# Performance work log

Hardware: AMD Instinct MI355X
Metric: run time of the kernel (lower is better)

## Reference

```python
import jax, jax.numpy as jnp
import numpy as np

B, S, E = 4, 4096, 1024
HEADS, WINDOW = 16, 128
HEAD_DIM = E // HEADS


def setup_inputs() -> dict:
    key = jax.random.key(0)
    ks = jax.random.split(key, 6)
    x = jax.random.normal(ks[0], (B, S, E), dtype=jnp.float32)
    attn_mask = jnp.ones((B, 1, S), dtype=jnp.float32)
    scale = 1.0 / np.sqrt(E)
    Wq = jax.random.normal(ks[1], (E, E), dtype=jnp.float32) * scale
    Wk = jax.random.normal(ks[2], (E, E), dtype=jnp.float32) * scale
    Wv = jax.random.normal(ks[3], (E, E), dtype=jnp.float32) * scale
    Wo = jax.random.normal(ks[4], (E, E), dtype=jnp.float32) * scale
    return {"x": x, "attn_mask": attn_mask, "Wq": Wq, "Wk": Wk, "Wv": Wv, "Wo": Wo}


def _look_around(t, axis_windows=2):
    # t: [..., nw, w, ...]; returns concat of windows [i-1, i, i+1] along the
    # intra-window axis, zero-padded at the boundaries.
    pad = [(0, 0)] * t.ndim
    pad[axis_windows] = (1, 1)
    tp = jnp.pad(t, pad)
    nw = t.shape[axis_windows]
    def sl(start):
        idx = [slice(None)] * t.ndim
        idx[axis_windows] = slice(start, start + nw)
        return tp[tuple(idx)]
    return jnp.concatenate([sl(0), sl(1), sl(2)], axis=axis_windows + 1)


def _local_attention(q, k, v, key_mask, window):
    # q,k,v: [b, h, n, d]; key_mask: [b, n] bool. Non-causal, look_backward=1,
    # look_forward=1 (lucidrains LocalAttention defaults for causal=False).
    b, h, n, d = q.shape
    nw = n // window
    scale = d ** -0.5
    qb = q.reshape(b, h, nw, window, d) * scale
    kb = k.reshape(b, h, nw, window, d)
    vb = v.reshape(b, h, nw, window, d)
    k_look = _look_around(kb, axis_windows=2)  # [b,h,nw,3w,d]
    v_look = _look_around(vb, axis_windows=2)
    # mask: user key mask AND in-bounds (padded boundary windows are invalid)
    mb = key_mask.reshape(b, nw, window)
    m_look = _look_around(mb, axis_windows=1)  # [b,nw,3w]
    m_look = m_look[:, None, :, None, :]       # [b,1,nw,1,3w]
    scores = jnp.einsum('bhnwd,bhnkd->bhnwk', qb, k_look)
    mask_value = -jnp.finfo(scores.dtype).max
    scores = jnp.where(m_look, scores, mask_value)
    attn = jax.nn.softmax(scores, axis=-1)
    out = jnp.einsum('bhnwk,bhnkd->bhnwd', attn, v_look)
    return out.reshape(b, h, n, d)


def reference(x, attn_mask, Wq, Wk, Wv, Wo):
    b, c, e = x.shape
    h, d = HEADS, HEAD_DIM
    q = jnp.einsum('bce,ef->bcf', x, Wq.T).reshape(b, c, h, d).transpose(0, 2, 1, 3)
    k = jnp.einsum('bce,ef->bcf', x, Wk.T).reshape(b, c, h, d).transpose(0, 2, 1, 3)
    v = jnp.einsum('bce,ef->bcf', x, Wv.T).reshape(b, c, h, d).transpose(0, 2, 1, 3)
    key_mask = attn_mask[:, 0, :] > 0  # [b, c] bool
    attended = _local_attention(q, k, v, key_mask, WINDOW)
    attended = attended.transpose(0, 2, 1, 3).reshape(b, c, h * d)
    return jnp.einsum('bcf,fe->bce', attended, Wo.T)
```

## Files before the change

kernel.cpp:

```cpp
#include <hip/hip_runtime.h>
#include <stdint.h>

typedef __bf16 bf16_t;
typedef __bf16 bf16x8 __attribute__((ext_vector_type(8)));
typedef __bf16 bf16x4 __attribute__((ext_vector_type(4)));
typedef float f32x4 __attribute__((ext_vector_type(4)));

__device__ __forceinline__ f32x4 mfma16(bf16x8 a, bf16x8 b, f32x4 c) {
  return __builtin_amdgcn_mfma_f32_16x16x32_bf16(a, b, c, 0, 0, 0);
}

__device__ __forceinline__ void g2l16(const void* g, void* l) {
  __builtin_amdgcn_global_load_lds((const __attribute__((address_space(1))) void*)g,
                                   (__attribute__((address_space(3))) void*)l, 16, 0, 0);
}

#define FENCE() asm volatile("" ::: "memory")

__global__ void __launch_bounds__(256) cvt_f32_bf16(const float* __restrict__ in,
                                                    bf16_t* __restrict__ out) {
  long i = ((long)blockIdx.x * 256 + threadIdx.x) * 8;
  float4 f0 = *(const float4*)(in + i);
  float4 f1 = *(const float4*)(in + i + 4);
  bf16x8 v;
  v[0] = (bf16_t)f0.x; v[1] = (bf16_t)f0.y; v[2] = (bf16_t)f0.z; v[3] = (bf16_t)f0.w;
  v[4] = (bf16_t)f1.x; v[5] = (bf16_t)f1.y; v[6] = (bf16_t)f1.z; v[7] = (bf16_t)f1.w;
  *(bf16x8*)(out + i) = v;
}

template <typename OutT>
__global__ void __launch_bounds__(512, 2) gemm256(const bf16_t* __restrict__ A,
                                                  const bf16_t* __restrict__ Bt,
                                                  OutT* __restrict__ C,
                                                  int M, int N, int K, int NBN) {
  extern __shared__ char smem[];
  const int t = threadIdx.x;
  const int w = t >> 6, l = t & 63;
  const int lr = l & 15, lg = l >> 4;
  const int wm = w >> 2, wn = w & 3;

  const int nwg = gridDim.x;
  const int flat = blockIdx.x;
  const int swz = (flat & 7) * (nwg >> 3) + (flat >> 3);
  const int bm = swz / NBN, bn = swz % NBN;
  const long rowA0 = (long)bm * 256;
  const long colC0 = (long)bn * 256;
  const int KT = K >> 6;

  const int colSwz = ((l & 7) ^ (l >> 3)) * 8;
  const bf16_t* gA = A + (rowA0 + w * 32 + (l >> 3)) * (long)K + colSwz;
  const bf16_t* gB = Bt + (colC0 + w * 32 + (l >> 3)) * (long)K + colSwz;
  const long K8 = (long)K * 8;

  const int sx0 = (lg ^ (lr & 7)) * 16;
  const int sx1 = ((4 + lg) ^ (lr & 7)) * 16;
  const int aRow = (wm * 128 + lr) * 128;
  const int bRow = 32768 + (wn * 64 + lr) * 128;

  f32x4 acc[8][4] = {};

#define STAGE_A(buf, kt)                                          \
  {                                                               \
    char* _d = smem + (buf) * 65536 + w * 4096;                   \
    const long _ko = (long)(kt) * 64;                             \
    g2l16(gA + _ko, _d);                                          \
    g2l16(gA + K8 + _ko, _d + 1024);                              \
    g2l16(gA + 2 * K8 + _ko, _d + 2048);                          \
    g2l16(gA + 3 * K8 + _ko, _d + 3072);                          \
  }
#define STAGE_B(buf, kt)                                          \
  {                                                               \
    char* _d = smem + (buf) * 65536 + 32768 + w * 4096;           \
    const long _ko = (long)(kt) * 64;                             \
    g2l16(gB + _ko, _d);                                          \
    g2l16(gB + K8 + _ko, _d + 1024);                              \
    g2l16(gB + 2 * K8 + _ko, _d + 2048);                          \
    g2l16(gB + 3 * K8 + _ko, _d + 3072);                          \
  }

  STAGE_A(0, 0); STAGE_B(0, 0);
  FENCE();
  asm volatile("s_waitcnt vmcnt(0)" ::: "memory");
  __builtin_amdgcn_s_barrier();

  for (int kt = 0; kt < KT; ++kt) {
    const char* sb = smem + (kt & 1) * 65536;
    const int nb = (kt + 1) & 1;
    const bool ds = (kt + 1) < KT;

    bf16x8 bfr[4][2];

    {
      bf16x8 a0[4][2];
#pragma unroll
      for (int j = 0; j < 4; ++j) {
        bfr[j][0] = *(const bf16x8*)(sb + bRow + j * 2048 + sx0);
        bfr[j][1] = *(const bf16x8*)(sb + bRow + j * 2048 + sx1);
      }
#pragma unroll
      for (int i = 0; i < 4; ++i) {
        a0[i][0] = *(const bf16x8*)(sb + aRow + i * 2048 + sx0);
        a0[i][1] = *(const bf16x8*)(sb + aRow + i * 2048 + sx1);
      }
      if (ds) STAGE_A(nb, kt + 1);
      FENCE();
      __builtin_amdgcn_s_barrier();
      asm volatile("s_waitcnt lgkmcnt(0)" ::: "memory");
      __builtin_amdgcn_sched_barrier(0);
      __builtin_amdgcn_s_setprio(1);
#pragma unroll
      for (int i = 0; i < 4; ++i)
#pragma unroll
        for (int j = 0; j < 4; ++j) {
          acc[i][j] = mfma16(a0[i][0], bfr[j][0], acc[i][j]);
          acc[i][j] = mfma16(a0[i][1], bfr[j][1], acc[i][j]);
        }
      __builtin_amdgcn_s_setprio(0);
      __builtin_amdgcn_sched_barrier(0);
      FENCE();
      __builtin_amdgcn_s_barrier();
    }

    {
      bf16x8 a1[4][2];
#pragma unroll
      for (int i = 0; i < 4; ++i) {
        a1[i][0] = *(const bf16x8*)(sb + aRow + (4 + i) * 2048 + sx0);
        a1[i][1] = *(const bf16x8*)(sb + aRow + (4 + i) * 2048 + sx1);
      }
      if (ds) STAGE_B(nb, kt + 1);
      FENCE();
      __builtin_amdgcn_s_barrier();
      asm volatile("s_waitcnt lgkmcnt(0)" ::: "memory");
      __builtin_amdgcn_sched_barrier(0);
      __builtin_amdgcn_s_setprio(1);
#pragma unroll
      for (int i = 0; i < 4; ++i)
#pragma unroll
        for (int j = 0; j < 4; ++j) {
          acc[4 + i][j] = mfma16(a1[i][0], bfr[j][0], acc[4 + i][j]);
          acc[4 + i][j] = mfma16(a1[i][1], bfr[j][1], acc[4 + i][j]);
        }
      __builtin_amdgcn_s_setprio(0);
      __builtin_amdgcn_sched_barrier(0);
      FENCE();
      if (ds) {
        asm volatile("s_waitcnt vmcnt(0)" ::: "memory");
      }
      __builtin_amdgcn_s_barrier();
    }
  }

#pragma unroll
  for (int i = 0; i < 8; ++i)
#pragma unroll
    for (int j = 0; j < 4; ++j)
#pragma unroll
      for (int r = 0; r < 4; ++r) {
        long row = rowA0 + wm * 128 + i * 16 + lg * 4 + r;
        long col = colC0 + wn * 64 + j * 16 + lr;
        C[row * (long)N + col] = (OutT)acc[i][j][r];
      }
#undef STAGE_A
#undef STAGE_B
}

__global__ void __launch_bounds__(512, 4) swa3(const bf16_t* __restrict__ QK,
                                               const bf16_t* __restrict__ VT,
                                               const float* __restrict__ amask,
                                               bf16_t* __restrict__ Att) {
  extern __shared__ char lds[];
  bf16_t* Ks = (bf16_t*)lds;
  bf16_t* Vs = (bf16_t*)(lds + 16384);
  float* bias = (float*)(lds + 32768);
  const int t = threadIdx.x, w = t >> 6, l = t & 63, lr = l & 15, lg = l >> 4;
  char* Psw = lds + 34304 + w * 4352;

  const int idx = (blockIdx.x & 7) * 256 + (blockIdx.x >> 3);
  const int n = idx & 31, h = (idx >> 5) & 15, b = idx >> 9;
  const long rowQ = (long)b * 4096 + n * 128;

  bf16x8 qf[2];
#pragma unroll
  for (int ks = 0; ks < 2; ++ks)
    qf[ks] = *(const bf16x8*)&QK[(rowQ + w * 16 + lr) * 2048 + h * 64 + ks * 32 + lg * 8];

  f32x4 oT[4] = {};
  float m_run = -1e30f, l_run = 0.f;

  const int kcLo = (n > 0) ? n - 1 : 0;
  const int kcHi = (n < 31) ? n + 1 : 31;
  const long kbase0 = (long)b * 4096 + (long)kcLo * 128;
  const int nch = kcHi - kcLo + 1;

  const int kcol = ((t & 7) ^ ((t >> 3) & 7)) * 8;
  const bf16_t* gK0 = QK + (kbase0 + (t >> 3)) * 2048 + 1024 + h * 64 + kcol;
  const int vrow = t >> 4;
  const int vcol = ((t & 15) ^ ((t >> 4) & 15)) * 8;
  const bf16_t* gV0 = VT + ((long)h * 64 + vrow) * 16384 + kbase0 + vcol;

  bf16_t* lK0 = Ks + t * 8;
  bf16_t* lK1 = Ks + 4096 + t * 8;
  bf16_t* lV0 = Vs + t * 8;
  bf16_t* lV1 = Vs + 4096 + t * 8;

#define STAGE_K(cc)                                               \
  {                                                               \
    const bf16_t* _k = gK0 + (long)(cc) * 128 * 2048;             \
    g2l16(_k, lK0);                                               \
    g2l16(_k + (long)64 * 2048, lK1);                             \
  }
#define STAGE_V(cc)                                               \
  {                                                               \
    const bf16_t* _v = gV0 + (long)(cc) * 128;                    \
    g2l16(_v, lV0);                                               \
    g2l16(_v + (long)32 * 16384, lV1);                            \
  }

  STAGE_K(0); STAGE_V(0);
  if (t < nch * 32) {
    float4 mv = *(const float4*)(amask + kbase0 + t * 4);
    float4 bv;
    bv.x = mv.x > 0.f ? 0.f : -1e30f;
    bv.y = mv.y > 0.f ? 0.f : -1e30f;
    bv.z = mv.z > 0.f ? 0.f : -1e30f;
    bv.w = mv.w > 0.f ? 0.f : -1e30f;
    *(float4*)&bias[t * 4] = bv;
  }
  FENCE();
  asm volatile("s_waitcnt vmcnt(0)" ::: "memory");
  __syncthreads();

  for (int c = 0; c < nch; ++c) {
    const bool more = (c + 1) < nch;

    f32x4 s[8];
#pragma unroll
    for (int kb = 0; kb < 8; ++kb) {
      f32x4 z = {};
#pragma unroll
      for (int ks = 0; ks < 2; ++ks) {
        bf16x8 kA = *(const bf16x8*)&Ks[(kb * 16 + lr) * 64 + (((ks * 4 + lg) ^ (lr & 7)) * 8)];
        z = mfma16(kA, qf[ks], z);
      }
      s[kb] = z;
    }
    FENCE();
    __builtin_amdgcn_s_barrier();
    if (more) STAGE_K(c + 1);

    float mt = -3e30f;
#pragma unroll
    for (int kb = 0; kb < 8; ++kb) {
      f32x4 bb = *(const f32x4*)&bias[c * 128 + kb * 16 + lg * 4];
#pragma unroll
      for (int r = 0; r < 4; ++r) {
        float sv = s[kb][r] * 0.125f + bb[r];
        s[kb][r] = sv;
        mt = fmaxf(mt, sv);
      }
    }
    mt = fmaxf(mt, __shfl_xor(mt, 16));
    mt = fmaxf(mt, __shfl_xor(mt, 32));
    float mnew = fmaxf(m_run, mt);
    float alpha = __expf(m_run - mnew);
    m_run = mnew;
    float rs = 0.f;
#pragma unroll
    for (int kb = 0; kb < 8; ++kb)
#pragma unroll
      for (int r = 0; r < 4; ++r) {
        float p = __expf(s[kb][r] - mnew);
        s[kb][r] = p;
        rs += p;
      }
    rs += __shfl_xor(rs, 16);
    rs += __shfl_xor(rs, 32);
    l_run = l_run * alpha + rs;
#pragma unroll
    for (int df = 0; df < 4; ++df)
#pragma unroll
      for (int r = 0; r < 4; ++r) oT[df][r] *= alpha;

#pragma unroll
    for (int kb = 0; kb < 8; ++kb) {
      bf16x4 pv;
      pv[0] = (bf16_t)s[kb][0]; pv[1] = (bf16_t)s[kb][1];
      pv[2] = (bf16_t)s[kb][2]; pv[3] = (bf16_t)s[kb][3];
      *(bf16x4*)(Psw + lr * 272 + kb * 32 + lg * 8) = pv;
    }
    asm volatile("s_waitcnt lgkmcnt(0)" ::: "memory");
    __builtin_amdgcn_sched_barrier(0);

    FENCE();
    if (more) asm volatile("s_waitcnt vmcnt(2)" ::: "memory");
    else      asm volatile("s_waitcnt vmcnt(0)" ::: "memory");
    __builtin_amdgcn_s_barrier();

#pragma unroll
    for (int ks = 0; ks < 4; ++ks) {
      bf16x8 pB = *(const bf16x8*)(Psw + lr * 272 + ks * 64 + lg * 16);
#pragma unroll
      for (int df = 0; df < 4; ++df) {
        bf16x8 vA = *(const bf16x8*)&Vs[(df * 16 + lr) * 128 + (((ks * 4 + lg) ^ lr) * 8)];
        oT[df] = mfma16(vA, pB, oT[df]);
      }
    }
    FENCE();
    __builtin_amdgcn_s_barrier();
    if (more) {
      STAGE_V(c + 1);
      FENCE();
      asm volatile("s_waitcnt vmcnt(2)" ::: "memory");
      __builtin_amdgcn_s_barrier();
    }
  }
#undef STAGE_K
#undef STAGE_V

  float inv = 1.f / l_run;
#pragma unroll
  for (int df = 0; df < 4; ++df) {
    bf16x4 ov;
#pragma unroll
    for (int r = 0; r < 4; ++r) ov[r] = (bf16_t)(oT[df][r] * inv);
    *(bf16x4*)(Psw + lr * 272 + df * 32 + lg * 8) = ov;
  }
  asm volatile("s_waitcnt lgkmcnt(0)" ::: "memory");
  __builtin_amdgcn_sched_barrier(0);
  const char* myP = lds + 34304 + w * 4352;
  bf16x8 r0 = *(const bf16x8*)(myP + (l >> 2) * 272 + (l & 3) * 32);
  bf16x8 r1 = *(const bf16x8*)(myP + (l >> 2) * 272 + (l & 3) * 32 + 16);
  long orow = rowQ + w * 16 + (l >> 2);
  bf16_t* op = Att + orow * 1024 + h * 64 + (l & 3) * 16;
  *(bf16x8*)op = r0;
  *(bf16x8*)(op + 8) = r1;
}

extern "C" void kernel_launch(void* const* d_in, const int* in_sizes, int n_in,
                              void* d_out, int out_size, void* d_ws, size_t ws_size,
                              hipStream_t stream) {
  const float* x  = (const float*)d_in[0];
  const float* am = (const float*)d_in[1];
  const float* Wq = (const float*)d_in[2];
  const float* Wk = (const float*)d_in[3];
  const float* Wv = (const float*)d_in[4];
  const float* Wo = (const float*)d_in[5];
  float* out = (float*)d_out;

  char* ws = (char*)d_ws;
  bf16_t* qk  = (bf16_t*)ws;
  bf16_t* vt  = (bf16_t*)(ws + 67108864);
  bf16_t* xbx = (bf16_t*)(ws + 100663296);
  bf16_t* wqk = (bf16_t*)(ws + 134217728);
  bf16_t* wvb = (bf16_t*)(ws + 138412032);
  bf16_t* wob = (bf16_t*)(ws + 140509184);

  const int kSmemG = 131072;
  hipFuncSetAttribute(reinterpret_cast<const void*>(&gemm256<bf16_t>),
                      hipFuncAttributeMaxDynamicSharedMemorySize, kSmemG);
  hipFuncSetAttribute(reinterpret_cast<const void*>(&gemm256<float>),
                      hipFuncAttributeMaxDynamicSharedMemorySize, kSmemG);
  const int kSmemS = 69120;
  hipFuncSetAttribute(reinterpret_cast<const void*>(&swa3),
                      hipFuncAttributeMaxDynamicSharedMemorySize, kSmemS);

  cvt_f32_bf16<<<8192, 256, 0, stream>>>(x, xbx);
  cvt_f32_bf16<<<512, 256, 0, stream>>>(Wq, wqk);
  cvt_f32_bf16<<<512, 256, 0, stream>>>(Wk, wqk + 1048576);
  cvt_f32_bf16<<<512, 256, 0, stream>>>(Wv, wvb);
  cvt_f32_bf16<<<512, 256, 0, stream>>>(Wo, wob);

  gemm256<bf16_t><<<512, 512, kSmemG, stream>>>(xbx, wqk, qk, 16384, 2048, 1024, 8);

  gemm256<bf16_t><<<256, 512, kSmemG, stream>>>(wvb, xbx, vt, 1024, 16384, 1024, 64);

  swa3<<<2048, 512, kSmemS, stream>>>(qk, vt, am, xbx);

  gemm256<float><<<256, 512, kSmemG, stream>>>(xbx, wob, out, 16384, 1024, 1024, 4);
}
```

Before: 229.7 us.

## Use triple-buffered K=32 LDS pipeline in GEMM with two tiles in flight

Rewrites the bf16 GEMM main loop from a double-buffered K=64 stage, split into two half-phases, to a three-slot ring of K=32 stages, prefetching two tiles ahead with vmcnt-based partial waits. Each iteration loads all A/B fragments once and issues 32 MFMAs between barriers. The goal is to hide global-load latency better and cut LDS from 128KB to 96KB. In exchange it has twice as many iterations, so barrier overhead per unit of work goes up, and a new swizzle pattern could change LDS bank conflicts.

```diff
diff --git a/kernel.cpp b/kernel.cpp
--- a/kernel.cpp
+++ b/kernel.cpp
@@ -29,10 +29,10 @@
 }
 
 template <typename OutT>
-__global__ void __launch_bounds__(512, 2) gemm256(const bf16_t* __restrict__ A,
-                                                  const bf16_t* __restrict__ Bt,
-                                                  OutT* __restrict__ C,
-                                                  int M, int N, int K, int NBN) {
+__global__ void __launch_bounds__(512, 2) gemm3r(const bf16_t* __restrict__ A,
+                                                 const bf16_t* __restrict__ Bt,
+                                                 OutT* __restrict__ C,
+                                                 int M, int N, int K, int NBN) {
   extern __shared__ char smem[];
   const int t = threadIdx.x;
   const int w = t >> 6, l = t & 63;
@@ -45,111 +45,66 @@
   const int bm = swz / NBN, bn = swz % NBN;
   const long rowA0 = (long)bm * 256;
   const long colC0 = (long)bn * 256;
-  const int KT = K >> 6;
-
-  const int colSwz = ((l & 7) ^ (l >> 3)) * 8;
-  const bf16_t* gA = A + (rowA0 + w * 32 + (l >> 3)) * (long)K + colSwz;
-  const bf16_t* gB = Bt + (colC0 + w * 32 + (l >> 3)) * (long)K + colSwz;
-  const long K8 = (long)K * 8;
-
-  const int sx0 = (lg ^ (lr & 7)) * 16;
-  const int sx1 = ((4 + lg) ^ (lr & 7)) * 16;
-  const int aRow = (wm * 128 + lr) * 128;
-  const int bRow = 32768 + (wn * 64 + lr) * 128;
+  const int KT = K >> 5;
+
+  const int colSwz = (((t & 3) ^ ((t >> 2) & 3))) * 8;
+  const bf16_t* gA = A + (rowA0 + (t >> 2)) * (long)K + colSwz;
+  const bf16_t* gB = Bt + (colC0 + (t >> 2)) * (long)K + colSwz;
+  const long K128 = (long)K * 128;
+
+  const int sxa = (lg ^ (lr & 3)) * 16;
+  const int aRow = (wm * 128 + lr) * 64;
+  const int bRow = 16384 + (wn * 64 + lr) * 64;
 
   f32x4 acc[8][4] = {};
 
-#define STAGE_A(buf, kt)                                          \
+#define STAGE(slot, kt)                                           \
   {                                                               \
-    char* _d = smem + (buf) * 65536 + w * 4096;                   \
-    const long _ko = (long)(kt) * 64;                             \
+    char* _d = smem + (slot) * 32768 + t * 16;                    \
+    const long _ko = (long)(kt) * 32;                             \
     g2l16(gA + _ko, _d);                                          \
-    g2l16(gA + K8 + _ko, _d + 1024);                              \
-    g2l16(gA + 2 * K8 + _ko, _d + 2048);                          \
-    g2l16(gA + 3 * K8 + _ko, _d + 3072);                          \
-  }
-#define STAGE_B(buf, kt)                                          \
-  {                                                               \
-    char* _d = smem + (buf) * 65536 + 32768 + w * 4096;           \
-    const long _ko = (long)(kt) * 64;                             \
-    g2l16(gB + _ko, _d);                                          \
-    g2l16(gB + K8 + _ko, _d + 1024);                              \
-    g2l16(gB + 2 * K8 + _ko, _d + 2048);                          \
-    g2l16(gB + 3 * K8 + _ko, _d + 3072);                          \
-  }
-
-  STAGE_A(0, 0); STAGE_B(0, 0);
+    g2l16(gA + K128 + _ko, _d + 8192);                            \
+    g2l16(gB + _ko, _d + 16384);                                  \
+    g2l16(gB + K128 + _ko, _d + 24576);                           \
+  }
+
+  STAGE(0, 0);
+  STAGE(1, 1);
   FENCE();
-  asm volatile("s_waitcnt vmcnt(0)" ::: "memory");
+  asm volatile("s_waitcnt vmcnt(4)" ::: "memory");
   __builtin_amdgcn_s_barrier();
 
   for (int kt = 0; kt < KT; ++kt) {
-    const char* sb = smem + (kt & 1) * 65536;
-    const int nb = (kt + 1) & 1;
-    const bool ds = (kt + 1) < KT;
-
-    bf16x8 bfr[4][2];
-
-    {
-      bf16x8 a0[4][2];
-#pragma unroll
-      for (int j = 0; j < 4; ++j) {
-        bfr[j][0] = *(const bf16x8*)(sb + bRow + j * 2048 + sx0);
-        bfr[j][1] = *(const bf16x8*)(sb + bRow + j * 2048 + sx1);
-      }
-#pragma unroll
-      for (int i = 0; i < 4; ++i) {
-        a0[i][0] = *(const bf16x8*)(sb + aRow + i * 2048 + sx0);
-        a0[i][1] = *(const bf16x8*)(sb + aRow + i * 2048 + sx1);
-      }
-      if (ds) STAGE_A(nb, kt + 1);
-      FENCE();
+    const char* sb = smem + (kt % 3) * 32768;
+
+    bf16x8 a[8], b[4];
+#pragma unroll
+    for (int j = 0; j < 4; ++j) b[j] = *(const bf16x8*)(sb + bRow + j * 1024 + sxa);
+#pragma unroll
+    for (int i = 0; i < 8; ++i) a[i] = *(const bf16x8*)(sb + aRow + i * 1024 + sxa);
+
+    if (kt + 2 < KT) STAGE((kt + 2) % 3, kt + 2);
+    FENCE();
+    __builtin_amdgcn_s_barrier();
+
+    __builtin_amdgcn_s_setprio(1);
+#pragma unroll
+    for (int i = 0; i < 8; ++i)
+#pragma unroll
+      for (int j = 0; j < 4; ++j) acc[i][j] = mfma16(a[i], b[j], acc[i][j]);
+    __builtin_amdgcn_s_setprio(0);
+    FENCE();
+
+    if (kt + 1 < KT) {
+      if (kt + 2 < KT) {
+        asm volatile("s_waitcnt vmcnt(4)" ::: "memory");
+      } else {
+        asm volatile("s_waitcnt vmcnt(0)" ::: "memory");
+      }
       __builtin_amdgcn_s_barrier();
-      asm volatile("s_waitcnt lgkmcnt(0)" ::: "memory");
-      __builtin_amdgcn_sched_barrier(0);
-      __builtin_amdgcn_s_setprio(1);
-#pragma unroll
-      for (int i = 0; i < 4; ++i)
-#pragma unroll
-        for (int j = 0; j < 4; ++j) {
-          acc[i][j] = mfma16(a0[i][0], bfr[j][0], acc[i][j]);
-          acc[i][j] = mfma16(a0[i][1], bfr[j][1], acc[i][j]);
-        }
-      __builtin_amdgcn_s_setprio(0);
-      __builtin_amdgcn_sched_barrier(0);
-      FENCE();
-      __builtin_amdgcn_s_barrier();
-    }
-
-    {
-      bf16x8 a1[4][2];
-#pragma unroll
-      for (int i = 0; i < 4; ++i) {
-        a1[i][0] = *(const bf16x8*)(sb + aRow + (4 + i) * 2048 + sx0);
-        a1[i][1] = *(const bf16x8*)(sb + aRow + (4 + i) * 2048 + sx1);
-      }
-      if (ds) STAGE_B(nb, kt + 1);
-      FENCE();
-      __builtin_amdgcn_s_barrier();
-      asm volatile("s_waitcnt lgkmcnt(0)" ::: "memory");
-      __builtin_amdgcn_sched_barrier(0);
-      __builtin_amdgcn_s_setprio(1);
-#pragma unroll
-      for (int i = 0; i < 4; ++i)
-#pragma unroll
-        for (int j = 0; j < 4; ++j) {
-          acc[4 + i][j] = mfma16(a1[i][0], bfr[j][0], acc[4 + i][j]);
-          acc[4 + i][j] = mfma16(a1[i][1], bfr[j][1], acc[4 + i][j]);
-        }
-      __builtin_amdgcn_s_setprio(0);
-      __builtin_amdgcn_sched_barrier(0);
-      FENCE();
-      if (ds) {
-        asm volatile("s_waitcnt vmcnt(0)" ::: "memory");
-      }
-      __builtin_amdgcn_s_barrier();
-    }
-  }
+    }
+  }
+#undef STAGE
 
 #pragma unroll
   for (int i = 0; i < 8; ++i)
@@ -161,8 +116,6 @@
         long col = colC0 + wn * 64 + j * 16 + lr;
         C[row * (long)N + col] = (OutT)acc[i][j][r];
       }
-#undef STAGE_A
-#undef STAGE_B
 }
 
 __global__ void __launch_bounds__(512, 4) swa3(const bf16_t* __restrict__ QK,
@@ -356,10 +309,10 @@
   bf16_t* wvb = (bf16_t*)(ws + 138412032);
   bf16_t* wob = (bf16_t*)(ws + 140509184);
 
-  const int kSmemG = 131072;
-  hipFuncSetAttribute(reinterpret_cast<const void*>(&gemm256<bf16_t>),
+  const int kSmemG = 98304;
+  hipFuncSetAttribute(reinterpret_cast<const void*>(&gemm3r<bf16_t>),
                       hipFuncAttributeMaxDynamicSharedMemorySize, kSmemG);
-  hipFuncSetAttribute(reinterpret_cast<const void*>(&gemm256<float>),
+  hipFuncSetAttribute(reinterpret_cast<const void*>(&gemm3r<float>),
                       hipFuncAttributeMaxDynamicSharedMemorySize, kSmemG);
   const int kSmemS = 69120;
   hipFuncSetAttribute(reinterpret_cast<const void*>(&swa3),
@@ -371,11 +324,11 @@
   cvt_f32_bf16<<<512, 256, 0, stream>>>(Wv, wvb);
   cvt_f32_bf16<<<512, 256, 0, stream>>>(Wo, wob);
 
-  gemm256<bf16_t><<<512, 512, kSmemG, stream>>>(xbx, wqk, qk, 16384, 2048, 1024, 8);
-
-  gemm256<bf16_t><<<256, 512, kSmemG, stream>>>(wvb, xbx, vt, 1024, 16384, 1024, 64);
+  gemm3r<bf16_t><<<512, 512, kSmemG, stream>>>(xbx, wqk, qk, 16384, 2048, 1024, 8);
+
+  gemm3r<bf16_t><<<256, 512, kSmemG, stream>>>(wvb, xbx, vt, 1024, 16384, 1024, 64);
 
   swa3<<<2048, 512, kSmemS, stream>>>(qk, vt, am, xbx);
 
-  gemm256<float><<<256, 512, kSmemG, stream>>>(xbx, wob, out, 16384, 1024, 1024, 4);
-}
+  gemm3r<float><<<256, 512, kSmemG, stream>>>(xbx, wob, out, 16384, 1024, 1024, 4);
+}
```

New measurement: 255.4 us. +11.2%, slower.

## Deepen GEMM prefetch by splitting tile loads into quarter-stages across sub-phases

Applied to the files above, without the earlier changes.

Reworks the GEMM main loop so the A and B tiles are each loaded in two halves. The next-next K tile's B halves and first A half are issued into the buffer being consumed, interleaved across four compute sub-phases, with partial vmcnt waits instead of a full drain. The aim is to keep more global-to-LDS traffic in flight and hide load latency behind MFMA work. In exchange it adds more barriers per iteration and more intricate buffer-reuse ordering, which risks races if the wait counts are off.

```diff
diff --git a/kernel.cpp b/kernel.cpp
--- a/kernel.cpp
+++ b/kernel.cpp
@@ -29,10 +29,10 @@
 }
 
 template <typename OutT>
-__global__ void __launch_bounds__(512, 2) gemm256(const bf16_t* __restrict__ A,
-                                                  const bf16_t* __restrict__ Bt,
-                                                  OutT* __restrict__ C,
-                                                  int M, int N, int K, int NBN) {
+__global__ void __launch_bounds__(512, 2) gemmC(const bf16_t* __restrict__ A,
+                                                const bf16_t* __restrict__ Bt,
+                                                OutT* __restrict__ C,
+                                                int M, int N, int K, int NBN) {
   extern __shared__ char smem[];
   const int t = threadIdx.x;
   const int w = t >> 6, l = t & 63;
@@ -47,10 +47,12 @@
   const long colC0 = (long)bn * 256;
   const int KT = K >> 6;
 
-  const int colSwz = ((l & 7) ^ (l >> 3)) * 8;
-  const bf16_t* gA = A + (rowA0 + w * 32 + (l >> 3)) * (long)K + colSwz;
-  const bf16_t* gB = Bt + (colC0 + w * 32 + (l >> 3)) * (long)K + colSwz;
-  const long K8 = (long)K * 8;
+  const int colSwz = ((t & 7) ^ ((t >> 3) & 7)) * 8;
+  const bf16_t* gA0 = A + (rowA0 + (t >> 3)) * (long)K + colSwz;
+  const bf16_t* gA1 = gA0 + (long)128 * K;
+  const bf16_t* gB0 = Bt + (colC0 + (t >> 3)) * (long)K + colSwz;
+  const bf16_t* gB1 = gB0 + (long)128 * K;
+  const long K64 = (long)K * 64;
 
   const int sx0 = (lg ^ (lr & 7)) * 16;
   const int sx1 = ((4 + lg) ^ (lr & 7)) * 16;
@@ -59,61 +61,62 @@
 
   f32x4 acc[8][4] = {};
 
-#define STAGE_A(buf, kt)                                          \
-  {                                                               \
-    char* _d = smem + (buf) * 65536 + w * 4096;                   \
-    const long _ko = (long)(kt) * 64;                             \
-    g2l16(gA + _ko, _d);                                          \
-    g2l16(gA + K8 + _ko, _d + 1024);                              \
-    g2l16(gA + 2 * K8 + _ko, _d + 2048);                          \
-    g2l16(gA + 3 * K8 + _ko, _d + 3072);                          \
-  }
-#define STAGE_B(buf, kt)                                          \
-  {                                                               \
-    char* _d = smem + (buf) * 65536 + 32768 + w * 4096;           \
-    const long _ko = (long)(kt) * 64;                             \
-    g2l16(gB + _ko, _d);                                          \
-    g2l16(gB + K8 + _ko, _d + 1024);                              \
-    g2l16(gB + 2 * K8 + _ko, _d + 2048);                          \
-    g2l16(gB + 3 * K8 + _ko, _d + 3072);                          \
-  }
-
-  STAGE_A(0, 0); STAGE_B(0, 0);
+#define ST_A0(buf, kt) {                                              \
+    char* _d = smem + (buf) * 65536 + t * 16;                         \
+    const bf16_t* _s = gA0 + (long)(kt) * 64;                         \
+    g2l16(_s, _d); g2l16(_s + K64, _d + 8192); }
+#define ST_A1(buf, kt) {                                              \
+    char* _d = smem + (buf) * 65536 + 16384 + t * 16;                 \
+    const bf16_t* _s = gA1 + (long)(kt) * 64;                         \
+    g2l16(_s, _d); g2l16(_s + K64, _d + 8192); }
+#define ST_B0(buf, kt) {                                              \
+    char* _d = smem + (buf) * 65536 + 32768 + t * 16;                 \
+    const bf16_t* _s = gB0 + (long)(kt) * 64;                         \
+    g2l16(_s, _d); g2l16(_s + K64, _d + 8192); }
+#define ST_B1(buf, kt) {                                              \
+    char* _d = smem + (buf) * 65536 + 49152 + t * 16;                 \
+    const bf16_t* _s = gB1 + (long)(kt) * 64;                         \
+    g2l16(_s, _d); g2l16(_s + K64, _d + 8192); }
+
+  ST_A0(0, 0); ST_A1(0, 0); ST_B0(0, 0); ST_B1(0, 0);
+  ST_B0(1, 1); ST_B1(1, 1); ST_A0(1, 1);
   FENCE();
-  asm volatile("s_waitcnt vmcnt(0)" ::: "memory");
+  asm volatile("s_waitcnt vmcnt(6)" ::: "memory");
   __builtin_amdgcn_s_barrier();
 
   for (int kt = 0; kt < KT; ++kt) {
     const char* sb = smem + (kt & 1) * 65536;
-    const int nb = (kt + 1) & 1;
-    const bool ds = (kt + 1) < KT;
+    const int nbuf = (kt + 1) & 1;
+    const int tbuf = kt & 1;
+    const bool s1 = (kt + 1) < KT;
+    const bool s2 = (kt + 2) < KT;
 
     bf16x8 bfr[4][2];
 
     {
-      bf16x8 a0[4][2];
+      bf16x8 ap[2][2];
 #pragma unroll
       for (int j = 0; j < 4; ++j) {
         bfr[j][0] = *(const bf16x8*)(sb + bRow + j * 2048 + sx0);
         bfr[j][1] = *(const bf16x8*)(sb + bRow + j * 2048 + sx1);
       }
 #pragma unroll
-      for (int i = 0; i < 4; ++i) {
-        a0[i][0] = *(const bf16x8*)(sb + aRow + i * 2048 + sx0);
-        a0[i][1] = *(const bf16x8*)(sb + aRow + i * 2048 + sx1);
-      }
-      if (ds) STAGE_A(nb, kt + 1);
+      for (int i = 0; i < 2; ++i) {
+        ap[i][0] = *(const bf16x8*)(sb + aRow + i * 2048 + sx0);
+        ap[i][1] = *(const bf16x8*)(sb + aRow + i * 2048 + sx1);
+      }
+      if (s1) ST_A1(nbuf, kt + 1);
       FENCE();
       __builtin_amdgcn_s_barrier();
       asm volatile("s_waitcnt lgkmcnt(0)" ::: "memory");
       __builtin_amdgcn_sched_barrier(0);
       __builtin_amdgcn_s_setprio(1);
 #pragma unroll
-      for (int i = 0; i < 4; ++i)
+      for (int i = 0; i < 2; ++i)
 #pragma unroll
         for (int j = 0; j < 4; ++j) {
-          acc[i][j] = mfma16(a0[i][0], bfr[j][0], acc[i][j]);
-          acc[i][j] = mfma16(a0[i][1], bfr[j][1], acc[i][j]);
+          acc[i][j] = mfma16(ap[i][0], bfr[j][0], acc[i][j]);
+          acc[i][j] = mfma16(ap[i][1], bfr[j][1], acc[i][j]);
         }
       __builtin_amdgcn_s_setprio(0);
       __builtin_amdgcn_sched_barrier(0);
@@ -121,35 +124,73 @@
       __builtin_amdgcn_s_barrier();
     }
 
-    {
-      bf16x8 a1[4][2];
-#pragma unroll
-      for (int i = 0; i < 4; ++i) {
-        a1[i][0] = *(const bf16x8*)(sb + aRow + (4 + i) * 2048 + sx0);
-        a1[i][1] = *(const bf16x8*)(sb + aRow + (4 + i) * 2048 + sx1);
-      }
-      if (ds) STAGE_B(nb, kt + 1);
+#pragma unroll
+    for (int p = 0; p < 2; ++p) {
+      bf16x8 ap[2][2];
+#pragma unroll
+      for (int i = 0; i < 2; ++i) {
+        ap[i][0] = *(const bf16x8*)(sb + aRow + (2 + 2 * p + i) * 2048 + sx0);
+        ap[i][1] = *(const bf16x8*)(sb + aRow + (2 + 2 * p + i) * 2048 + sx1);
+      }
+      if (s2) {
+        if (p == 0) { ST_B0(tbuf, kt + 2); }
+        else        { ST_B1(tbuf, kt + 2); }
+      }
       FENCE();
       __builtin_amdgcn_s_barrier();
       asm volatile("s_waitcnt lgkmcnt(0)" ::: "memory");
       __builtin_amdgcn_sched_barrier(0);
       __builtin_amdgcn_s_setprio(1);
 #pragma unroll
-      for (int i = 0; i < 4; ++i)
+      for (int i = 0; i < 2; ++i)
 #pragma unroll
         for (int j = 0; j < 4; ++j) {
-          acc[4 + i][j] = mfma16(a1[i][0], bfr[j][0], acc[4 + i][j]);
-          acc[4 + i][j] = mfma16(a1[i][1], bfr[j][1], acc[4 + i][j]);
+          acc[2 + 2 * p + i][j] = mfma16(ap[i][0], bfr[j][0], acc[2 + 2 * p + i][j]);
+          acc[2 + 2 * p + i][j] = mfma16(ap[i][1], bfr[j][1], acc[2 + 2 * p + i][j]);
         }
       __builtin_amdgcn_s_setprio(0);
       __builtin_amdgcn_sched_barrier(0);
       FENCE();
-      if (ds) {
+      __builtin_amdgcn_s_barrier();
+    }
+
+    {
+      bf16x8 ap[2][2];
+#pragma unroll
+      for (int i = 0; i < 2; ++i) {
+        ap[i][0] = *(const bf16x8*)(sb + aRow + (6 + i) * 2048 + sx0);
+        ap[i][1] = *(const bf16x8*)(sb + aRow + (6 + i) * 2048 + sx1);
+      }
+      FENCE();
+      __builtin_amdgcn_s_barrier();
+      asm volatile("s_waitcnt lgkmcnt(0)" ::: "memory");
+      __builtin_amdgcn_sched_barrier(0);
+      __builtin_amdgcn_s_setprio(1);
+#pragma unroll
+      for (int i = 0; i < 2; ++i)
+#pragma unroll
+        for (int j = 0; j < 4; ++j) {
+          acc[6 + i][j] = mfma16(ap[i][0], bfr[j][0], acc[6 + i][j]);
+          acc[6 + i][j] = mfma16(ap[i][1], bfr[j][1], acc[6 + i][j]);
+        }
+      __builtin_amdgcn_s_setprio(0);
+      __builtin_amdgcn_sched_barrier(0);
+      FENCE();
+      if (s2) {
+        ST_A0(tbuf, kt + 2);
+        FENCE();
+        asm volatile("s_waitcnt vmcnt(6)" ::: "memory");
+        __builtin_amdgcn_s_barrier();
+      } else if (s1) {
         asm volatile("s_waitcnt vmcnt(0)" ::: "memory");
-      }
-      __builtin_amdgcn_s_barrier();
-    }
-  }
+        __builtin_amdgcn_s_barrier();
+      }
+    }
+  }
+#undef ST_A0
+#undef ST_A1
+#undef ST_B0
+#undef ST_B1
 
 #pragma unroll
   for (int i = 0; i < 8; ++i)
@@ -161,8 +202,6 @@
         long col = colC0 + wn * 64 + j * 16 + lr;
         C[row * (long)N + col] = (OutT)acc[i][j][r];
       }
-#undef STAGE_A
-#undef STAGE_B
 }
 
 __global__ void __launch_bounds__(512, 4) swa3(const bf16_t* __restrict__ QK,
@@ -357,9 +396,9 @@
   bf16_t* wob = (bf16_t*)(ws + 140509184);
 
   const int kSmemG = 131072;
-  hipFuncSetAttribute(reinterpret_cast<const void*>(&gemm256<bf16_t>),
+  hipFuncSetAttribute(reinterpret_cast<const void*>(&gemmC<bf16_t>),
                       hipFuncAttributeMaxDynamicSharedMemorySize, kSmemG);
-  hipFuncSetAttribute(reinterpret_cast<const void*>(&gemm256<float>),
+  hipFuncSetAttribute(reinterpret_cast<const void*>(&gemmC<float>),
                       hipFuncAttributeMaxDynamicSharedMemorySize, kSmemG);
   const int kSmemS = 69120;
   hipFuncSetAttribute(reinterpret_cast<const void*>(&swa3),
@@ -371,11 +410,11 @@
   cvt_f32_bf16<<<512, 256, 0, stream>>>(Wv, wvb);
   cvt_f32_bf16<<<512, 256, 0, stream>>>(Wo, wob);
 
-  gemm256<bf16_t><<<512, 512, kSmemG, stream>>>(xbx, wqk, qk, 16384, 2048, 1024, 8);
-
-  gemm256<bf16_t><<<256, 512, kSmemG, stream>>>(wvb, xbx, vt, 1024, 16384, 1024, 64);
+  gemmC<bf16_t><<<512, 512, kSmemG, stream>>>(xbx, wqk, qk, 16384, 2048, 1024, 8);
+
+  gemmC<bf16_t><<<256, 512, kSmemG, stream>>>(wvb, xbx, vt, 1024, 16384, 1024, 64);
 
   swa3<<<2048, 512, kSmemS, stream>>>(qk, vt, am, xbx);
 
-  gemm256<float><<<256, 512, kSmemG, stream>>>(xbx, wob, out, 16384, 1024, 1024, 4);
-}
+  gemmC<float><<<256, 512, kSmemG, stream>>>(xbx, wob, out, 16384, 1024, 1024, 4);
+}
```

After: 235.4 us. 2.5% more time.

## Fuse weight casts and QK/VT GEMMs, drop online-softmax max tracking

Applied to the files above, without the earlier changes.

The four weight-conversion launches become one kernel, and the separate QK and V-transpose GEMMs run as a single 768-block launch through a shared device-side GEMM core. Together these cut launch overhead and let the smaller GEMM fill the larger one's tail. In the sliding-window attention kernel, the running max and rescaling are removed. Probabilities are computed directly as exp2 of the scaled score plus the mask bias, which saves reductions, shuffles and accumulator rescales per chunk. The risk is overflow if scores grow large, since no max is subtracted anymore.

```diff
diff --git a/kernel.cpp b/kernel.cpp
--- a/kernel.cpp
+++ b/kernel.cpp
@@ -28,20 +28,42 @@
   *(bf16x8*)(out + i) = v;
 }
 
+__global__ void __launch_bounds__(256) cvt_weights(const float* __restrict__ Wq,
+                                                   const float* __restrict__ Wk,
+                                                   const float* __restrict__ Wv,
+                                                   const float* __restrict__ Wo,
+                                                   bf16_t* __restrict__ wqk,
+                                                   bf16_t* __restrict__ wvb,
+                                                   bf16_t* __restrict__ wob) {
+  const int id = blockIdx.x;
+  const int seg = id >> 9, off = id & 511;
+  const float* src;
+  bf16_t* dst;
+  if (seg == 0)      { src = Wq; dst = wqk; }
+  else if (seg == 1) { src = Wk; dst = wqk + 1048576; }
+  else if (seg == 2) { src = Wv; dst = wvb; }
+  else               { src = Wo; dst = wob; }
+  long i = ((long)off * 256 + threadIdx.x) * 8;
+  float4 f0 = *(const float4*)(src + i);
+  float4 f1 = *(const float4*)(src + i + 4);
+  bf16x8 v;
+  v[0] = (bf16_t)f0.x; v[1] = (bf16_t)f0.y; v[2] = (bf16_t)f0.z; v[3] = (bf16_t)f0.w;
+  v[4] = (bf16_t)f1.x; v[5] = (bf16_t)f1.y; v[6] = (bf16_t)f1.z; v[7] = (bf16_t)f1.w;
+  *(bf16x8*)(dst + i) = v;
+}
+
 template <typename OutT>
-__global__ void __launch_bounds__(512, 2) gemm256(const bf16_t* __restrict__ A,
-                                                  const bf16_t* __restrict__ Bt,
-                                                  OutT* __restrict__ C,
-                                                  int M, int N, int K, int NBN) {
-  extern __shared__ char smem[];
+__device__ __forceinline__ void gemm_core(const bf16_t* __restrict__ A,
+                                          const bf16_t* __restrict__ Bt,
+                                          OutT* __restrict__ C,
+                                          int N, int K, int NBN, int nseg, int flat,
+                                          char* smem) {
   const int t = threadIdx.x;
   const int w = t >> 6, l = t & 63;
   const int lr = l & 15, lg = l >> 4;
   const int wm = w >> 2, wn = w & 3;
 
-  const int nwg = gridDim.x;
-  const int flat = blockIdx.x;
-  const int swz = (flat & 7) * (nwg >> 3) + (flat >> 3);
+  const int swz = (flat & 7) * (nseg >> 3) + (flat >> 3);
   const int bm = swz / NBN, bn = swz % NBN;
   const long rowA0 = (long)bm * 256;
   const long colC0 = (long)bn * 256;
@@ -150,6 +172,8 @@
       __builtin_amdgcn_s_barrier();
     }
   }
+#undef STAGE_A
+#undef STAGE_B
 
 #pragma unroll
   for (int i = 0; i < 8; ++i)
@@ -161,8 +185,27 @@
         long col = colC0 + wn * 64 + j * 16 + lr;
         C[row * (long)N + col] = (OutT)acc[i][j][r];
       }
-#undef STAGE_A
-#undef STAGE_B
+}
+
+__global__ void __launch_bounds__(512, 2) gemm_qkvt(const bf16_t* __restrict__ xb,
+                                                    const bf16_t* __restrict__ wqk,
+                                                    bf16_t* __restrict__ qk,
+                                                    const bf16_t* __restrict__ wvb,
+                                                    bf16_t* __restrict__ vt) {
+  extern __shared__ char smem[];
+  const int id = blockIdx.x;
+  if (id < 512) {
+    gemm_core<bf16_t>(xb, wqk, qk, 2048, 1024, 8, 512, id, smem);
+  } else {
+    gemm_core<bf16_t>(wvb, xb, vt, 16384, 1024, 64, 256, id - 512, smem);
+  }
+}
+
+__global__ void __launch_bounds__(512, 2) gemm_out(const bf16_t* __restrict__ att,
+                                                   const bf16_t* __restrict__ wob,
+                                                   float* __restrict__ out) {
+  extern __shared__ char smem[];
+  gemm_core<float>(att, wob, out, 1024, 1024, 4, 256, blockIdx.x, smem);
 }
 
 __global__ void __launch_bounds__(512, 4) swa3(const bf16_t* __restrict__ QK,
@@ -186,7 +229,7 @@
     qf[ks] = *(const bf16x8*)&QK[(rowQ + w * 16 + lr) * 2048 + h * 64 + ks * 32 + lg * 8];
 
   f32x4 oT[4] = {};
-  float m_run = -1e30f, l_run = 0.f;
+  float l_run = 0.f;
 
   const int kcLo = (n > 0) ? n - 1 : 0;
   const int kcHi = (n < 31) ? n + 1 : 31;
@@ -231,6 +274,8 @@
   asm volatile("s_waitcnt vmcnt(0)" ::: "memory");
   __syncthreads();
 
+  const float c1 = 0.18033688011112042f;
+
   for (int c = 0; c < nch; ++c) {
     const bool more = (c + 1) < nch;
 
@@ -249,38 +294,20 @@
     __builtin_amdgcn_s_barrier();
     if (more) STAGE_K(c + 1);
 
-    float mt = -3e30f;
+    float rs = 0.f;
 #pragma unroll
     for (int kb = 0; kb < 8; ++kb) {
       f32x4 bb = *(const f32x4*)&bias[c * 128 + kb * 16 + lg * 4];
 #pragma unroll
       for (int r = 0; r < 4; ++r) {
-        float sv = s[kb][r] * 0.125f + bb[r];
-        s[kb][r] = sv;
-        mt = fmaxf(mt, sv);
-      }
-    }
-    mt = fmaxf(mt, __shfl_xor(mt, 16));
-    mt = fmaxf(mt, __shfl_xor(mt, 32));
-    float mnew = fmaxf(m_run, mt);
-    float alpha = __expf(m_run - mnew);
-    m_run = mnew;
-    float rs = 0.f;
-#pragma unroll
-    for (int kb = 0; kb < 8; ++kb)
-#pragma unroll
-      for (int r = 0; r < 4; ++r) {
-        float p = __expf(s[kb][r] - mnew);
+        float p = __builtin_amdgcn_exp2f(s[kb][r] * c1 + bb[r]);
         s[kb][r] = p;
         rs += p;
       }
+    }
     rs += __shfl_xor(rs, 16);
     rs += __shfl_xor(rs, 32);
-    l_run = l_run * alpha + rs;
-#pragma unroll
-    for (int df = 0; df < 4; ++df)
-#pragma unroll
-      for (int r = 0; r < 4; ++r) oT[df][r] *= alpha;
+    l_run += rs;
 
 #pragma unroll
     for (int kb = 0; kb < 8; ++kb) {
@@ -357,25 +384,20 @@
   bf16_t* wob = (bf16_t*)(ws + 140509184);
 
   const int kSmemG = 131072;
-  hipFuncSetAttribute(reinterpret_cast<const void*>(&gemm256<bf16_t>),
+  hipFuncSetAttribute(reinterpret_cast<const void*>(&gemm_qkvt),
                       hipFuncAttributeMaxDynamicSharedMemorySize, kSmemG);
-  hipFuncSetAttribute(reinterpret_cast<const void*>(&gemm256<float>),
+  hipFuncSetAttribute(reinterpret_cast<const void*>(&gemm_out),
                       hipFuncAttributeMaxDynamicSharedMemorySize, kSmemG);
   const int kSmemS = 69120;
   hipFuncSetAttribute(reinterpret_cast<const void*>(&swa3),
                       hipFuncAttributeMaxDynamicSharedMemorySize, kSmemS);
 
   cvt_f32_bf16<<<8192, 256, 0, stream>>>(x, xbx);
-  cvt_f32_bf16<<<512, 256, 0, stream>>>(Wq, wqk);
-  cvt_f32_bf16<<<512, 256, 0, stream>>>(Wk, wqk + 1048576);
-  cvt_f32_bf16<<<512, 256, 0, stream>>>(Wv, wvb);
-  cvt_f32_bf16<<<512, 256, 0, stream>>>(Wo, wob);
-
-  gemm256<bf16_t><<<512, 512, kSmemG, stream>>>(xbx, wqk, qk, 16384, 2048, 1024, 8);
-
-  gemm256<bf16_t><<<256, 512, kSmemG, stream>>>(wvb, xbx, vt, 1024, 16384, 1024, 64);
+  cvt_weights<<<2048, 256, 0, stream>>>(Wq, Wk, Wv, Wo, wqk, wvb, wob);
+
+  gemm_qkvt<<<768, 512, kSmemG, stream>>>(xbx, wqk, qk, wvb, vt);
 
   swa3<<<2048, 512, kSmemS, stream>>>(qk, vt, am, xbx);
 
-  gemm256<float><<<256, 512, kSmemG, stream>>>(xbx, wob, out, 16384, 1024, 1024, 4);
-}
+  gemm_out<<<256, 512, kSmemG, stream>>>(xbx, wob, out);
+}
```

Result: faster. 212.9 us (-7.3%).
